# Performance work log

Hardware: AMD Instinct MI355X
Metric: run time of the kernel (lower is better)

The kernel has to match this reference:

```python
import jax, jax.numpy as jnp
import numpy as np

B = 512
IN_F, HID, OUT_F = 342, 512, 311


def setup_inputs() -> dict:
    key = jax.random.key(0)
    ks = jax.random.split(key, 8)
    return {
        "p": jax.random.uniform(ks[0], (B,), dtype=jnp.float32),
        "x": jax.random.normal(ks[1], (B, IN_F), dtype=jnp.float32),
        "W0": jax.random.normal(ks[2], (4, IN_F, HID), dtype=jnp.float32) * 0.05,
        "b0": jax.random.normal(ks[3], (4, HID), dtype=jnp.float32) * 0.05,
        "W1": jax.random.normal(ks[4], (4, HID, HID), dtype=jnp.float32) * 0.05,
        "b1": jax.random.normal(ks[5], (4, HID), dtype=jnp.float32) * 0.05,
        "W2": jax.random.normal(ks[6], (4, HID, OUT_F), dtype=jnp.float32) * 0.05,
        "b2": jax.random.normal(ks[7], (4, OUT_F), dtype=jnp.float32) * 0.05,
    }


def _cubic(y0, y1, y2, y3, mu, mu2, mu3):
    # Catmull-Rom cubic interpolation (same coefficients as the torch module)
    return ((-0.5 * y0 + 1.5 * y1 - 1.5 * y2 + 0.5 * y3) * mu3
            + (y0 - 2.5 * y1 + 2.0 * y2 - 0.5 * y3) * mu2
            + (-0.5 * y0 + 0.5 * y2) * mu
            + y1)


def reference(p, x, W0, b0, W1, b1, W2, b2):
    p4 = p * 4.0
    pa = jnp.mod(p4, 1.0)                      # (B,) fractional phase
    i1 = p4.astype(jnp.int32) % 4              # (B,) control point indices
    i0 = (i1 - 1) % 4
    i2 = (i1 + 1) % 4
    i3 = (i1 + 2) % 4

    wa = pa[:, None, None]                     # (B,1,1) for weights
    wa2, wa3 = wa * wa, wa * wa * wa
    ba = pa[:, None]                           # (B,1) for biases
    ba2, ba3 = ba * ba, ba * ba * ba

    def interp_w(W):  # W: (4, din, dout) -> (B, din, dout)
        return _cubic(W[i0], W[i1], W[i2], W[i3], wa, wa2, wa3)

    def interp_b(b):  # b: (4, d) -> (B, d)
        return _cubic(b[i0], b[i1], b[i2], b[i3], ba, ba2, ba3)

    h = jax.nn.elu(jnp.einsum('bi,bio->bo', x, interp_w(W0)) + interp_b(b0))
    h = jax.nn.elu(jnp.einsum('bi,bio->bo', h, interp_w(W1)) + interp_b(b1))
    y = jnp.einsum('bi,bio->bo', h, interp_w(W2)) + interp_b(b2)
    return y
```

## Files before the change

kernel.cpp:

```cpp
#include <hip/hip_runtime.h>
#include <math.h>

typedef __bf16 bf16x8 __attribute__((ext_vector_type(8)));
typedef float f32x4 __attribute__((ext_vector_type(4)));

#define B_SZ 512
#define IN_F 342
#define HID  512
#define OUT_F 311

template <int JOB>
__device__ void wt_transpose(const float* __restrict__ W, __bf16* __restrict__ T,
                             int t) {
  constexpr int KP   = (JOB == 0) ? 384 : 512;
  constexpr int KWF  = (JOB == 0) ? IN_F : HID;
  constexpr int NC   = (JOB == 2) ? OUT_F : HID;
  constexpr int NSUB = (JOB == 2) ? 320 : 512;
  constexpr int KT   = KP / 64;
  const int r0 = (t / KT) * 64, k0 = (t % KT) * 64;
  __shared__ __bf16 tile[64][66];
  const int tid = threadIdx.x;
  const int rl = tid & 63;
  const int c = r0 / NSUB;
  const int nbase = r0 - c * NSUB;
#pragma unroll
  for (int jj = 0; jj < 16; ++jj) {
    int kl = (tid >> 6) + jj * 4;
    int k = k0 + kl;
    int n = nbase + rl;
    float v = 0.0f;
    if ((JOB != 0 || k < KWF) && (JOB != 2 || n < NC))
      v = W[((size_t)c * KWF + k) * NC + n];
    tile[rl][kl] = (__bf16)v;
  }
  __syncthreads();
  int row = tid >> 2, o0 = (tid & 3) * 16;
  bf16x8 v0 = *(const bf16x8*)&tile[row][o0];
  bf16x8 v1 = *(const bf16x8*)&tile[row][o0 + 8];
  int g = (nbase + row) * 4 + c;
  __bf16* dst = T + (size_t)g * KP + k0 + o0;
  *(bf16x8*)dst = v0;
  *(bf16x8*)(dst + 8) = v1;
}

template <int LAYER>
__device__ void gemm_body(int nx, int my, const __bf16* __restrict__ A,
                          const __bf16* __restrict__ BT,
                          const float* __restrict__ bias,
                          const float* __restrict__ coef,
                          void* __restrict__ outv) {
  constexpr int KA = (LAYER == 0) ? 384 : 512;
  constexpr int T = KA / 64;
  constexpr int LDT = 72;
  __shared__ __bf16 Als[32 * LDT];
  __shared__ __bf16 Bls[64 * LDT];

  const int tid = threadIdx.x;
  const int l = tid & 63;
  const int wave = tid >> 6;
  const int wm = wave >> 1, wn = wave & 1;
  const int lr = l & 15, lk = l >> 4;
  const int m0 = my * 32;
  const int n0 = nx * 64;

  const int ar = tid >> 3, ao = tid & 7;
  const int br = tid >> 2, bo = (tid & 3) * 2;

  const __bf16* Ap = A + (size_t)(m0 + ar) * KA + ao * 8;
  const __bf16* Bp = BT + (size_t)(n0 + br) * KA + bo * 8;

  bf16x8 a0_, b0_, b1_;
  bf16x8 a1_, b2_, b3_;
  f32x4 acc[2] = {};

  auto load0 = [&](int t) {
    a0_ = *(const bf16x8*)&Ap[t * 64];
    b0_ = *(const bf16x8*)&Bp[t * 64];
    b1_ = *(const bf16x8*)&Bp[t * 64 + 8];
  };
  auto load1 = [&](int t) {
    a1_ = *(const bf16x8*)&Ap[t * 64];
    b2_ = *(const bf16x8*)&Bp[t * 64];
    b3_ = *(const bf16x8*)&Bp[t * 64 + 8];
  };
  auto store0 = [&]() {
    *(bf16x8*)&Als[ar * LDT + ao * 8] = a0_;
    *(bf16x8*)&Bls[br * LDT + bo * 8] = b0_;
    *(bf16x8*)&Bls[br * LDT + bo * 8 + 8] = b1_;
  };
  auto store1 = [&]() {
    *(bf16x8*)&Als[ar * LDT + ao * 8] = a1_;
    *(bf16x8*)&Bls[br * LDT + bo * 8] = b2_;
    *(bf16x8*)&Bls[br * LDT + bo * 8 + 8] = b3_;
  };
  auto compute = [&]() {
#pragma unroll
    for (int kk = 0; kk < 64; kk += 32) {
      bf16x8 af = *(const bf16x8*)&Als[(wm * 16 + lr) * LDT + kk + lk * 8];
      bf16x8 bg[2];
#pragma unroll
      for (int j = 0; j < 2; ++j)
        bg[j] = *(const bf16x8*)&Bls[(wn * 32 + j * 16 + lr) * LDT + kk + lk * 8];
#pragma unroll
      for (int j = 0; j < 2; ++j)
        acc[j] = __builtin_amdgcn_mfma_f32_16x16x32_bf16(af, bg[j], acc[j], 0, 0, 0);
    }
  };

  load0(0);
  load1(1);
  for (int t = 0; t < T; t += 2) {
    __syncthreads();
    store0();
    __syncthreads();
    if (t + 2 < T) load0(t + 2);
    compute();
    __syncthreads();
    store1();
    __syncthreads();
    if (t + 3 < T) load1(t + 3);
    compute();
  }

  const int cl = l & 3;
#pragma unroll
  for (int j = 0; j < 2; ++j) {
    int gnp = n0 + wn * 32 + j * 16 + lr;
    int hn = gnp >> 2;
    float bv;
    if (LAYER == 2) bv = (hn < OUT_F) ? bias[cl * OUT_F + hn] : 0.0f;
    else            bv = bias[cl * HID + hn];
#pragma unroll
    for (int r = 0; r < 4; ++r) {
      int gm = m0 + wm * 16 + lk * 4 + r;
      float cf = coef[gm * 4 + cl];
      float v = cf * (acc[j][r] + bv);
      v += __shfl_xor(v, 1);
      v += __shfl_xor(v, 2);
      if (LAYER == 2) {
        if (cl == 0 && hn < OUT_F)
          ((float*)outv)[(size_t)gm * OUT_F + hn] = v;
      } else {
        if (cl == 0) {
          float e = (v > 0.0f) ? v : expm1f(v);
          ((__bf16*)outv)[(size_t)gm * HID + hn] = (__bf16)e;
        }
      }
    }
  }
}

__global__ __launch_bounds__(256) void setup_kernel(
    const float* __restrict__ p, const float* __restrict__ x,
    const float* __restrict__ W0, const float* __restrict__ W1,
    const float* __restrict__ W2, float* __restrict__ coef,
    __bf16* __restrict__ A0, __bf16* __restrict__ T0,
    __bf16* __restrict__ T1, __bf16* __restrict__ T2) {
  int bid = blockIdx.x, tid = threadIdx.x;
  if (bid < 192)      { wt_transpose<0>(W0, T0, bid); return; }
  if (bid < 448)      { wt_transpose<1>(W1, T1, bid - 192); return; }
  if (bid < 608)      { wt_transpose<2>(W2, T2, bid - 448); return; }
  if (bid < 624) {
    int base = (bid - 608) * 32;
    for (int e = tid; e < 32 * 384; e += 256) {
      int m = base + e / 384, i = e - (e / 384) * 384;
      A0[(size_t)m * 384 + i] =
          (i < IN_F) ? (__bf16)x[(size_t)m * IN_F + i] : (__bf16)0.0f;
    }
    return;
  }
  for (int b = tid; b < B_SZ; b += 256) {
    float p4 = p[b] * 4.0f;
    float mu = p4 - floorf(p4);
    int i1 = ((int)p4) & 3;
    float mu2 = mu * mu, mu3 = mu2 * mu;
    float c0 = -0.5f * mu3 + mu2 - 0.5f * mu;
    float c1 =  1.5f * mu3 - 2.5f * mu2 + 1.0f;
    float c2 = -1.5f * mu3 + 2.0f * mu2 + 0.5f * mu;
    float c3 =  0.5f * mu3 - 0.5f * mu2;
    float arr[4];
    arr[(i1 + 3) & 3] = c0;
    arr[i1]           = c1;
    arr[(i1 + 1) & 3] = c2;
    arr[(i1 + 2) & 3] = c3;
    coef[b * 4 + 0] = arr[0];
    coef[b * 4 + 1] = arr[1];
    coef[b * 4 + 2] = arr[2];
    coef[b * 4 + 3] = arr[3];
  }
}

__global__ __launch_bounds__(256) void g0_kernel(
    const __bf16* __restrict__ A0, const __bf16* __restrict__ T0,
    const float* __restrict__ b0, const float* __restrict__ coef,
    __bf16* __restrict__ E1) {
  gemm_body<0>(blockIdx.x, blockIdx.y, A0, T0, b0, coef, E1);
}

__global__ __launch_bounds__(256) void g1_kernel(
    const __bf16* __restrict__ E1, const __bf16* __restrict__ T1,
    const float* __restrict__ b1, const float* __restrict__ coef,
    __bf16* __restrict__ E2) {
  gemm_body<1>(blockIdx.x, blockIdx.y, E1, T1, b1, coef, E2);
}

__global__ __launch_bounds__(256) void g2_kernel(
    const __bf16* __restrict__ E2, const __bf16* __restrict__ T2,
    const float* __restrict__ b2, const float* __restrict__ coef,
    float* __restrict__ out) {
  gemm_body<2>(blockIdx.x, blockIdx.y, E2, T2, b2, coef, out);
}

extern "C" void kernel_launch(void* const* d_in, const int* in_sizes, int n_in,
                              void* d_out, int out_size, void* d_ws, size_t ws_size,
                              hipStream_t stream) {
  const float* p  = (const float*)d_in[0];
  const float* x  = (const float*)d_in[1];
  const float* W0 = (const float*)d_in[2];
  const float* b0 = (const float*)d_in[3];
  const float* W1 = (const float*)d_in[4];
  const float* b1 = (const float*)d_in[5];
  const float* W2 = (const float*)d_in[6];
  const float* b2 = (const float*)d_in[7];
  float* out = (float*)d_out;

  char* w = (char*)d_ws;
  float*  coef = (float*)w;   w += 8192;
  __bf16* A0   = (__bf16*)w;  w += (size_t)B_SZ * 384 * 2;
  __bf16* T0   = (__bf16*)w;  w += (size_t)2048 * 384 * 2;
  __bf16* T1   = (__bf16*)w;  w += (size_t)2048 * 512 * 2;
  __bf16* T2   = (__bf16*)w;  w += (size_t)1280 * 512 * 2;
  __bf16* E1   = (__bf16*)w;  w += (size_t)B_SZ * HID * 2;
  __bf16* E2   = (__bf16*)w;  w += (size_t)B_SZ * HID * 2;

  setup_kernel<<<625, 256, 0, stream>>>(p, x, W0, W1, W2, coef, A0, T0, T1, T2);
  g0_kernel<<<dim3(32, 16), 256, 0, stream>>>(A0, T0, b0, coef, E1);
  g1_kernel<<<dim3(32, 16), 256, 0, stream>>>(E1, T1, b1, coef, E2);
  g2_kernel<<<dim3(20, 16), 256, 0, stream>>>(E2, T2, b2, coef, out);
}
```

Baseline: 43.41 us.

## Double-buffer LDS with 128-wide K tiles and one barrier per step

The GEMM main loop moves from 64-wide K steps with a single LDS buffer and four barriers per two steps to 128-wide K steps with ping-pong LDS buffers and one barrier per step. Global loads for the next tile are issued before computing the current one, then stored to the alternate buffer. The aim is fewer synchronisations and better overlap of memory with MFMA work. In exchange it roughly doubles LDS use per block, which may reduce occupancy, and the layer-0 loop has only three iterations.

```diff
diff --git a/kernel.cpp b/kernel.cpp
--- a/kernel.cpp
+++ b/kernel.cpp
@@ -50,10 +50,12 @@
                           const float* __restrict__ coef,
                           void* __restrict__ outv) {
   constexpr int KA = (LAYER == 0) ? 384 : 512;
-  constexpr int T = KA / 64;
-  constexpr int LDT = 72;
-  __shared__ __bf16 Als[32 * LDT];
-  __shared__ __bf16 Bls[64 * LDT];
+  constexpr int T = KA / 128;
+  constexpr int LDA = 136;
+  constexpr int ASZ = 32 * LDA;
+  constexpr int BSZ = 64 * LDA;
+  __shared__ __bf16 Als[2 * ASZ];
+  __shared__ __bf16 Bls[2 * BSZ];
 
   const int tid = threadIdx.x;
   const int l = tid & 63;
@@ -64,62 +66,58 @@
   const int n0 = nx * 64;
 
   const int ar = tid >> 3, ao = tid & 7;
-  const int br = tid >> 2, bo = (tid & 3) * 2;
+  const int br = tid >> 2, bo = tid & 3;
 
   const __bf16* Ap = A + (size_t)(m0 + ar) * KA + ao * 8;
-  const __bf16* Bp = BT + (size_t)(n0 + br) * KA + bo * 8;
-
-  bf16x8 a0_, b0_, b1_;
-  bf16x8 a1_, b2_, b3_;
+  const __bf16* Bp = BT + (size_t)(n0 + br) * KA + bo * 16;
+
+  bf16x8 a0_, a1_, b0_, b1_, b2_, b3_;
   f32x4 acc[2] = {};
 
-  auto load0 = [&](int t) {
-    a0_ = *(const bf16x8*)&Ap[t * 64];
-    b0_ = *(const bf16x8*)&Bp[t * 64];
-    b1_ = *(const bf16x8*)&Bp[t * 64 + 8];
+  auto loadreg = [&](int t) {
+    a0_ = *(const bf16x8*)&Ap[t * 128];
+    a1_ = *(const bf16x8*)&Ap[t * 128 + 64];
+    b0_ = *(const bf16x8*)&Bp[t * 128];
+    b1_ = *(const bf16x8*)&Bp[t * 128 + 8];
+    b2_ = *(const bf16x8*)&Bp[t * 128 + 64];
+    b3_ = *(const bf16x8*)&Bp[t * 128 + 72];
   };
-  auto load1 = [&](int t) {
-    a1_ = *(const bf16x8*)&Ap[t * 64];
-    b2_ = *(const bf16x8*)&Bp[t * 64];
-    b3_ = *(const bf16x8*)&Bp[t * 64 + 8];
+  auto storeLDS = [&](int ph) {
+    __bf16* Ac = Als + ph * ASZ;
+    __bf16* Bc = Bls + ph * BSZ;
+    *(bf16x8*)&Ac[ar * LDA + ao * 8] = a0_;
+    *(bf16x8*)&Ac[ar * LDA + ao * 8 + 64] = a1_;
+    *(bf16x8*)&Bc[br * LDA + bo * 16] = b0_;
+    *(bf16x8*)&Bc[br * LDA + bo * 16 + 8] = b1_;
+    *(bf16x8*)&Bc[br * LDA + bo * 16 + 64] = b2_;
+    *(bf16x8*)&Bc[br * LDA + bo * 16 + 72] = b3_;
   };
-  auto store0 = [&]() {
-    *(bf16x8*)&Als[ar * LDT + ao * 8] = a0_;
-    *(bf16x8*)&Bls[br * LDT + bo * 8] = b0_;
-    *(bf16x8*)&Bls[br * LDT + bo * 8 + 8] = b1_;
-  };
-  auto store1 = [&]() {
-    *(bf16x8*)&Als[ar * LDT + ao * 8] = a1_;
-    *(bf16x8*)&Bls[br * LDT + bo * 8] = b2_;
-    *(bf16x8*)&Bls[br * LDT + bo * 8 + 8] = b3_;
-  };
-  auto compute = [&]() {
-#pragma unroll
-    for (int kk = 0; kk < 64; kk += 32) {
-      bf16x8 af = *(const bf16x8*)&Als[(wm * 16 + lr) * LDT + kk + lk * 8];
+  auto compute = [&](int ph) {
+    const __bf16* Ac = Als + ph * ASZ;
+    const __bf16* Bc = Bls + ph * BSZ;
+#pragma unroll
+    for (int kk = 0; kk < 128; kk += 32) {
+      bf16x8 af = *(const bf16x8*)&Ac[(wm * 16 + lr) * LDA + kk + lk * 8];
       bf16x8 bg[2];
 #pragma unroll
       for (int j = 0; j < 2; ++j)
-        bg[j] = *(const bf16x8*)&Bls[(wn * 32 + j * 16 + lr) * LDT + kk + lk * 8];
+        bg[j] = *(const bf16x8*)&Bc[(wn * 32 + j * 16 + lr) * LDA + kk + lk * 8];
 #pragma unroll
       for (int j = 0; j < 2; ++j)
         acc[j] = __builtin_amdgcn_mfma_f32_16x16x32_bf16(af, bg[j], acc[j], 0, 0, 0);
     }
   };
 
-  load0(0);
-  load1(1);
-  for (int t = 0; t < T; t += 2) {
-    __syncthreads();
-    store0();
-    __syncthreads();
-    if (t + 2 < T) load0(t + 2);
-    compute();
-    __syncthreads();
-    store1();
-    __syncthreads();
-    if (t + 3 < T) load1(t + 3);
-    compute();
+  loadreg(0);
+  storeLDS(0);
+  __syncthreads();
+  for (int t = 0; t < T; ++t) {
+    if (t + 1 < T) loadreg(t + 1);
+    compute(t & 1);
+    if (t + 1 < T) {
+      storeLDS((t + 1) & 1);
+      __syncthreads();
+    }
   }
 
   const int cl = l & 3;
```

Result: faster. 42.45 us (-2.2%).
